# Performance work log

Hardware: AMD Instinct MI355X
Metric: run time of the kernel (lower is better)

The kernel has to match this reference:

```python
import jax, jax.numpy as jnp
import numpy as np

B, N, D = 2, 2048, 1024
H = 16
HD = D // H
SCALE = HD ** -0.5


def setup_inputs() -> dict:
    key = jax.random.key(0)
    k1, k2, kw, kb = jax.random.split(key, 4)
    x1 = jax.random.normal(k1, (B, N, D), dtype=jnp.float32)
    x2 = jax.random.normal(k2, (B, N, D), dtype=jnp.float32)
    # fused qkv linear: torch nn.Linear(dim, 3*dim): W [3D, D], b [3D]
    bound = 1.0 / np.sqrt(D)
    qkv_w = jax.random.uniform(kw, (3 * D, D), minval=-bound, maxval=bound, dtype=jnp.float32)
    qkv_b = jax.random.uniform(kb, (3 * D,), minval=-bound, maxval=bound, dtype=jnp.float32)
    return {"x1": x1, "x2": x2, "qkv_w": qkv_w, "qkv_b": qkv_b}


def reference(x1, x2, qkv_w, qkv_b):
    # qkv projections (only q from x1 and k,v from x2 are used by the module)
    q1 = (jnp.einsum('bnd,ed->bne', x1, qkv_w[:D]) + qkv_b[:D])
    k2 = (jnp.einsum('bnd,ed->bne', x2, qkv_w[D:2 * D]) + qkv_b[D:2 * D])
    v2 = (jnp.einsum('bnd,ed->bne', x2, qkv_w[2 * D:]) + qkv_b[2 * D:])
    # [B, H, N, HD]
    q1 = q1.reshape(B, N, H, HD).transpose(0, 2, 1, 3)
    k2 = k2.reshape(B, N, H, HD).transpose(0, 2, 1, 3)
    v2 = v2.reshape(B, N, H, HD).transpose(0, 2, 1, 3)
    # explicit QK^T -> softmax -> AV (materializes [B,H,N,N] like the original)
    scores = jnp.einsum('bhqd,bhkd->bhqk', q1, k2) * SCALE
    attn = jax.nn.softmax(scores, axis=-1)
    out = jnp.einsum('bhqk,bhkd->bhqd', attn, v2)
    # [B, N, D]; note original module skips out_proj (never applied in forward)
    return out.transpose(0, 2, 1, 3).reshape(B, N, D)
```

## Files before the change

kernel.cpp:

```cpp
#include <hip/hip_runtime.h>
#include <cstdint>
#include <cstddef>

#define B_   2
#define N_   2048
#define D_   1024
#define H_   16
#define HD_  64
#define QSCALE_ 0.18033688011112042f

typedef unsigned short u16;
typedef unsigned int   u32;
typedef __attribute__((ext_vector_type(8))) short short8;
typedef __attribute__((ext_vector_type(4))) float f32x4;
typedef __attribute__((ext_vector_type(4))) float fl4;
typedef __attribute__((ext_vector_type(4))) unsigned short us4;

__device__ __forceinline__ u16 f2bf(float f) {
  u32 u = __builtin_bit_cast(u32, f);
  u += 0x7fffu + ((u >> 16) & 1u);
  return (u16)(u >> 16);
}

__device__ __forceinline__ void gload16(const void* g, void* l) {
  typedef __attribute__((address_space(1))) unsigned int gu32;
  typedef __attribute__((address_space(3))) unsigned int lu32;
  __builtin_amdgcn_global_load_lds((gu32*)g, (lu32*)l, 16, 0, 0);
}

__global__ void convert_kernel(const fl4* __restrict__ x1, const fl4* __restrict__ x2,
                               const fl4* __restrict__ w,
                               us4* __restrict__ o1, us4* __restrict__ o2,
                               us4* __restrict__ ow) {
  const int NX = (B_ * N_ * D_) / 4;
  const int NW = (3 * D_ * D_) / 4;
  int stride = gridDim.x * blockDim.x;
  for (int i = blockIdx.x * blockDim.x + threadIdx.x; i < NX; i += stride) {
    fl4 a = x1[i];
    us4 r; r.x = f2bf(a.x); r.y = f2bf(a.y); r.z = f2bf(a.z); r.w = f2bf(a.w);
    o1[i] = r;
    fl4 b = x2[i];
    us4 s; s.x = f2bf(b.x); s.y = f2bf(b.y); s.z = f2bf(b.z); s.w = f2bf(b.w);
    o2[i] = s;
    if (i < NW) {
      fl4 c = w[i];
      us4 t; t.x = f2bf(c.x); t.y = f2bf(c.y); t.z = f2bf(c.z); t.w = f2bf(c.w);
      ow[i] = t;
    }
  }
}

__global__ __launch_bounds__(256) void qkv_gemm(
    const u16* __restrict__ x1b, const u16* __restrict__ x2b,
    const u16* __restrict__ wb, const float* __restrict__ bias,
    u16* __restrict__ Qb, u16* __restrict__ Kb, u16* __restrict__ Vcb) {
  const int z = blockIdx.z;
  const u16* X = (z == 0) ? x1b : x2b;
  const u16* W = wb + (size_t)z * D_ * D_;
  const float* bz = bias + z * D_;
  const int m0 = blockIdx.y * 128;
  const int e0 = blockIdx.x * 128;
  const int tid = threadIdx.x;
  const int lane = tid & 63;
  const int w = tid >> 6;
  const int wr = w >> 1, wc = w & 1;
  const int col = lane & 15, quad = lane >> 4;

  __shared__ __align__(16) u16 As[128 * 32];
  __shared__ __align__(16) u16 Bs[128 * 32];
  __shared__ __align__(16) u16 Tb[4][16 * 72];

  f32x4 acc[4][4] = {};

  int off0 = w * 2048 + lane * 16;
  int row0 = off0 >> 6;
  int ke0  = (off0 & 63) >> 1;
  int off1 = off0 + 1024;
  int row1 = off1 >> 6;
  int ke1  = (off1 & 63) >> 1;

  const u16* gA0 = X + (size_t)(m0 + row0) * D_ + ke0;
  const u16* gA1 = X + (size_t)(m0 + row1) * D_ + ke1;
  const u16* gB0 = W + (size_t)(e0 + row0) * D_ + ke0;
  const u16* gB1 = W + (size_t)(e0 + row1) * D_ + ke1;
  u16* lA0 = &As[w * 1024];
  u16* lA1 = &As[w * 1024 + 512];
  u16* lB0 = &Bs[w * 1024];
  u16* lB1 = &Bs[w * 1024 + 512];

  for (int k0 = 0; k0 < D_; k0 += 32) {
    __syncthreads();
    gload16(gA0 + k0, lA0);
    gload16(gA1 + k0, lA1);
    gload16(gB0 + k0, lB0);
    gload16(gB1 + k0, lB1);
    __syncthreads();

    short8 a[4], b[4];
#pragma unroll
    for (int i = 0; i < 4; ++i)
      a[i] = *(const short8*)&As[(wr * 64 + i * 16 + col) * 32 + quad * 8];
#pragma unroll
    for (int j = 0; j < 4; ++j)
      b[j] = *(const short8*)&Bs[(wc * 64 + j * 16 + col) * 32 + quad * 8];
#pragma unroll
    for (int i = 0; i < 4; ++i)
#pragma unroll
      for (int j = 0; j < 4; ++j)
        acc[i][j] = __builtin_amdgcn_mfma_f32_16x16x32_bf16(a[i], b[j], acc[i][j], 0, 0, 0);
  }

  if (z == 2) {
#pragma unroll
    for (int j = 0; j < 4; ++j) {
      int eg = e0 + wc * 64 + j * 16 + col;
      float bj = bz[eg];
      int h = eg >> 6, d = eg & 63;
#pragma unroll
      for (int i = 0; i < 4; ++i) {
        int m  = m0 + wr * 64 + i * 16 + quad * 4;
        int bb = m >> 11;
        int nc = (m & (N_ - 1)) >> 6;
        int no = i * 16 + quad * 4;
        int p  = (no >> 3) ^ (d & 7);
        us4 pk;
#pragma unroll
        for (int r = 0; r < 4; ++r) pk[r] = f2bf(acc[i][j][r] + bj);
        *(us4*)&Vcb[((((size_t)bb * H_ + h) * (N_ / 64) + nc) * HD_ + d) * 64
                    + p * 8 + (no & 7)] = pk;
      }
    }
  } else {
    u16* Tw = Tb[w];
    const int h = (e0 + wc * 64) >> 6;
    const int mb = m0 + wr * 64;
    const int bb = mb >> 11;
    const int nb = mb & (N_ - 1);
    float bjv[4];
#pragma unroll
    for (int j = 0; j < 4; ++j) bjv[j] = bz[e0 + wc * 64 + j * 16 + col];

    const int trow = lane >> 2;
    const int tchk = lane & 3;
#pragma unroll
    for (int i = 0; i < 4; ++i) {
#pragma unroll
      for (int j = 0; j < 4; ++j)
#pragma unroll
        for (int r = 0; r < 4; ++r) {
          float v = acc[i][j][r] + bjv[j];
          if (z == 0) v *= QSCALE_;
          Tw[(quad * 4 + r) * 72 + j * 16 + col] = f2bf(v);
        }
      __asm__ volatile("" ::: "memory");
      int n = nb + i * 16 + trow;
      size_t base = (((size_t)bb * H_ + h) * N_ + n) * HD_;
#pragma unroll
      for (int pass = 0; pass < 2; ++pass) {
        short8 vv = *(const short8*)&Tw[trow * 72 + tchk * 8 + pass * 32];
        if (z == 0) {
          *(short8*)&Qb[base + tchk * 8 + pass * 32] = vv;
        } else {
          int p = (tchk + 4 * pass) ^ (n & 7);
          *(short8*)&Kb[base + p * 8] = vv;
        }
      }
      __asm__ volatile("" ::: "memory");
    }
  }
}

__global__ __launch_bounds__(256, 3) void attn_kernel(
    const u16* __restrict__ Qb, const u16* __restrict__ Kb,
    const u16* __restrict__ Vcb, float* __restrict__ out) {
  const int bh = blockIdx.y;
  const int bb = bh >> 4, h = bh & 15;
  const int q0 = blockIdx.x * 128;
  const int tid = threadIdx.x;
  const int lane = tid & 63;
  const int w = tid >> 6;
  const int col = lane & 15, quad = lane >> 4;

  const u16* __restrict__ Q  = Qb  + ((size_t)bh << 17);
  const u16* __restrict__ Kg = Kb  + ((size_t)bh << 17);
  const u16* __restrict__ Vg = Vcb + ((size_t)bh << 17);

  __shared__ __align__(16) u16 Ks[2][64 * 64];
  __shared__ __align__(16) u16 Vs[2][64 * 64];
  __shared__ __align__(16) u16 P[4][32 * 72];
  u16* Pw = P[w];

  short8 qa[2][2];
#pragma unroll
  for (int m = 0; m < 2; ++m) {
    int qrow = q0 + w * 32 + m * 16 + col;
    qa[m][0] = *(const short8*)&Q[qrow * HD_ + quad * 8];
    qa[m][1] = *(const short8*)&Q[qrow * HD_ + 32 + quad * 8];
  }

  const int soff = (tid >> 3) * 64 + (tid & 7) * 8;

  f32x4 accO[2][4] = {};
  float lsum[2][4] = {};
  const int swz = col & 7;

  {
    const u16* gk = Kg + soff;
    const u16* gv = Vg + soff;
    gload16(gk,        &Ks[0][soff]);
    gload16(gk + 2048, &Ks[0][soff + 2048]);
    gload16(gv,        &Vs[0][soff]);
    gload16(gv + 2048, &Vs[0][soff + 2048]);
  }

  for (int it = 0; it < N_ / 64; ++it) {
    const int buf = it & 1;
    __syncthreads();
    if (it + 1 < N_ / 64) {
      const int k0 = (it + 1) * 64;
      const u16* gk = Kg + k0 * 64 + soff;
      const u16* gv = Vg + k0 * 64 + soff;
      gload16(gk,        &Ks[buf ^ 1][soff]);
      gload16(gk + 2048, &Ks[buf ^ 1][soff + 2048]);
      gload16(gv,        &Vs[buf ^ 1][soff]);
      gload16(gv + 2048, &Vs[buf ^ 1][soff + 2048]);
    }

    const u16* Kt = Ks[buf];
    f32x4 s[2][4] = {};
#pragma unroll
    for (int jn = 0; jn < 4; ++jn) {
      int base = (jn * 16 + col) * 64 + ((quad ^ swz) * 8);
      short8 kb0 = *(const short8*)&Kt[base];
      short8 kb1 = *(const short8*)&Kt[base ^ 32];
#pragma unroll
      for (int m = 0; m < 2; ++m) {
        s[m][jn] = __builtin_amdgcn_mfma_f32_16x16x32_bf16(qa[m][0], kb0, s[m][jn], 0, 0, 0);
        s[m][jn] = __builtin_amdgcn_mfma_f32_16x16x32_bf16(qa[m][1], kb1, s[m][jn], 0, 0, 0);
      }
    }

#pragma unroll
    for (int m = 0; m < 2; ++m)
#pragma unroll
      for (int jn = 0; jn < 4; ++jn)
#pragma unroll
        for (int r = 0; r < 4; ++r) {
          float e = exp2f(s[m][jn][r]);
          lsum[m][r] += e;
          Pw[(m * 16 + quad * 4 + r) * 72 + jn * 16 + col] =
              (u16)(__builtin_bit_cast(u32, e) >> 16);
        }
    __asm__ volatile("" ::: "memory");
    short8 pa[2][2];
#pragma unroll
    for (int m = 0; m < 2; ++m) {
      pa[m][0] = *(const short8*)&Pw[(m * 16 + col) * 72 + quad * 8];
      pa[m][1] = *(const short8*)&Pw[(m * 16 + col) * 72 + 32 + quad * 8];
    }
    __asm__ volatile("" ::: "memory");

    const u16* Vt = Vs[buf];
#pragma unroll
    for (int jd = 0; jd < 4; ++jd) {
      int base = (jd * 16 + col) * 64 + ((quad ^ swz) * 8);
      short8 vb0 = *(const short8*)&Vt[base];
      short8 vb1 = *(const short8*)&Vt[base ^ 32];
#pragma unroll
      for (int m = 0; m < 2; ++m) {
        accO[m][jd] = __builtin_amdgcn_mfma_f32_16x16x32_bf16(pa[m][0], vb0, accO[m][jd], 0, 0, 0);
        accO[m][jd] = __builtin_amdgcn_mfma_f32_16x16x32_bf16(pa[m][1], vb1, accO[m][jd], 0, 0, 0);
      }
    }
  }

#pragma unroll
  for (int m = 0; m < 2; ++m)
#pragma unroll
    for (int r = 0; r < 4; ++r) {
      float v = lsum[m][r];
      v += __shfl_xor(v, 1);
      v += __shfl_xor(v, 2);
      v += __shfl_xor(v, 4);
      v += __shfl_xor(v, 8);
      lsum[m][r] = 1.0f / v;
    }

#pragma unroll
  for (int m = 0; m < 2; ++m)
#pragma unroll
    for (int jd = 0; jd < 4; ++jd)
#pragma unroll
      for (int r = 0; r < 4; ++r) {
        int n = q0 + w * 32 + m * 16 + quad * 4 + r;
        int e = h * HD_ + jd * 16 + col;
        out[((size_t)bb * N_ + n) * D_ + e] = accO[m][jd][r] * lsum[m][r];
      }
}

extern "C" void kernel_launch(void* const* d_in, const int* in_sizes, int n_in,
                              void* d_out, int out_size, void* d_ws, size_t ws_size,
                              hipStream_t stream) {
  const float* x1 = (const float*)d_in[0];
  const float* x2 = (const float*)d_in[1];
  const float* qw = (const float*)d_in[2];
  const float* qb = (const float*)d_in[3];
  float* out = (float*)d_out;

  u16* ws   = (u16*)d_ws;
  u16* x1b  = ws;
  u16* x2b  = ws + 4194304;
  u16* wb   = ws + 8388608;
  u16* Qbf  = ws + 11534336;
  u16* Kbf  = ws + 15728640;
  u16* Vcb  = ws + 19922944;
  if (ws_size < (size_t)24117248 * 2) return;

  convert_kernel<<<dim3(1024), dim3(256), 0, stream>>>(
      (const fl4*)x1, (const fl4*)x2, (const fl4*)qw,
      (us4*)x1b, (us4*)x2b, (us4*)wb);

  qkv_gemm<<<dim3(8, 32, 3), dim3(256), 0, stream>>>(
      x1b, x2b, wb, qb, Qbf, Kbf, Vcb);

  attn_kernel<<<dim3(16, 32), dim3(256), 0, stream>>>(Qbf, Kbf, Vcb, out);
}
```

Measured before the change: 208.4 us.

## Use two waves with 64 query rows each in attention, and native exp2

The attention block shrinks from four waves to two. Each wave now covers 64 query rows (4 m-tiles), so every K/V fragment read from shared memory feeds twice as many MFMAs. The K/V tile loads are redistributed across 128 threads, and exp2f is replaced by the hardware v_exp_f32 instruction to skip libm range handling. In exchange, register pressure roughly doubles for the accumulators, and there are fewer waves per block to hide latency, which the launch bounds reflect.

```diff
diff --git a/kernel.cpp b/kernel.cpp
--- a/kernel.cpp
+++ b/kernel.cpp
@@ -20,6 +20,16 @@
   u32 u = __builtin_bit_cast(u32, f);
   u += 0x7fffu + ((u >> 16) & 1u);
   return (u16)(u >> 16);
+}
+
+__device__ __forceinline__ float fexp2(float x) {
+#if __has_builtin(__builtin_amdgcn_exp2f)
+  return __builtin_amdgcn_exp2f(x);
+#else
+  float r;
+  asm("v_exp_f32 %0, %1" : "=v"(r) : "v"(x));
+  return r;
+#endif
 }
 
 __device__ __forceinline__ void gload16(const void* g, void* l) {
@@ -170,7 +180,7 @@
   }
 }
 
-__global__ __launch_bounds__(256, 3) void attn_kernel(
+__global__ __launch_bounds__(128, 2) void attn_kernel(
     const u16* __restrict__ Qb, const u16* __restrict__ Kb,
     const u16* __restrict__ Vcb, float* __restrict__ out) {
   const int bh = blockIdx.y;
@@ -187,30 +197,27 @@
 
   __shared__ __align__(16) u16 Ks[2][64 * 64];
   __shared__ __align__(16) u16 Vs[2][64 * 64];
-  __shared__ __align__(16) u16 P[4][32 * 72];
+  __shared__ __align__(16) u16 P[2][64 * 72];
   u16* Pw = P[w];
 
-  short8 qa[2][2];
-#pragma unroll
-  for (int m = 0; m < 2; ++m) {
-    int qrow = q0 + w * 32 + m * 16 + col;
+  short8 qa[4][2];
+#pragma unroll
+  for (int m = 0; m < 4; ++m) {
+    int qrow = q0 + w * 64 + m * 16 + col;
     qa[m][0] = *(const short8*)&Q[qrow * HD_ + quad * 8];
     qa[m][1] = *(const short8*)&Q[qrow * HD_ + 32 + quad * 8];
   }
 
-  const int soff = (tid >> 3) * 64 + (tid & 7) * 8;
-
-  f32x4 accO[2][4] = {};
-  float lsum[2][4] = {};
+  const int soff = tid * 8;
+
+  f32x4 accO[4][4] = {};
+  float lsum[4][4] = {};
   const int swz = col & 7;
 
-  {
-    const u16* gk = Kg + soff;
-    const u16* gv = Vg + soff;
-    gload16(gk,        &Ks[0][soff]);
-    gload16(gk + 2048, &Ks[0][soff + 2048]);
-    gload16(gv,        &Vs[0][soff]);
-    gload16(gv + 2048, &Vs[0][soff + 2048]);
+#pragma unroll
+  for (int s = 0; s < 4; ++s) {
+    gload16(Kg + soff + s * 1024, &Ks[0][soff + s * 1024]);
+    gload16(Vg + soff + s * 1024, &Vs[0][soff + s * 1024]);
   }
 
   for (int it = 0; it < N_ / 64; ++it) {
@@ -220,41 +227,42 @@
       const int k0 = (it + 1) * 64;
       const u16* gk = Kg + k0 * 64 + soff;
       const u16* gv = Vg + k0 * 64 + soff;
-      gload16(gk,        &Ks[buf ^ 1][soff]);
-      gload16(gk + 2048, &Ks[buf ^ 1][soff + 2048]);
-      gload16(gv,        &Vs[buf ^ 1][soff]);
-      gload16(gv + 2048, &Vs[buf ^ 1][soff + 2048]);
+#pragma unroll
+      for (int s = 0; s < 4; ++s) {
+        gload16(gk + s * 1024, &Ks[buf ^ 1][soff + s * 1024]);
+        gload16(gv + s * 1024, &Vs[buf ^ 1][soff + s * 1024]);
+      }
     }
 
     const u16* Kt = Ks[buf];
-    f32x4 s[2][4] = {};
+    f32x4 s[4][4] = {};
 #pragma unroll
     for (int jn = 0; jn < 4; ++jn) {
       int base = (jn * 16 + col) * 64 + ((quad ^ swz) * 8);
       short8 kb0 = *(const short8*)&Kt[base];
       short8 kb1 = *(const short8*)&Kt[base ^ 32];
 #pragma unroll
-      for (int m = 0; m < 2; ++m) {
+      for (int m = 0; m < 4; ++m) {
         s[m][jn] = __builtin_amdgcn_mfma_f32_16x16x32_bf16(qa[m][0], kb0, s[m][jn], 0, 0, 0);
         s[m][jn] = __builtin_amdgcn_mfma_f32_16x16x32_bf16(qa[m][1], kb1, s[m][jn], 0, 0, 0);
       }
     }
 
 #pragma unroll
-    for (int m = 0; m < 2; ++m)
+    for (int m = 0; m < 4; ++m)
 #pragma unroll
       for (int jn = 0; jn < 4; ++jn)
 #pragma unroll
         for (int r = 0; r < 4; ++r) {
-          float e = exp2f(s[m][jn][r]);
+          float e = fexp2(s[m][jn][r]);
           lsum[m][r] += e;
           Pw[(m * 16 + quad * 4 + r) * 72 + jn * 16 + col] =
               (u16)(__builtin_bit_cast(u32, e) >> 16);
         }
     __asm__ volatile("" ::: "memory");
-    short8 pa[2][2];
-#pragma unroll
-    for (int m = 0; m < 2; ++m) {
+    short8 pa[4][2];
+#pragma unroll
+    for (int m = 0; m < 4; ++m) {
       pa[m][0] = *(const short8*)&Pw[(m * 16 + col) * 72 + quad * 8];
       pa[m][1] = *(const short8*)&Pw[(m * 16 + col) * 72 + 32 + quad * 8];
     }
@@ -267,7 +275,7 @@
       short8 vb0 = *(const short8*)&Vt[base];
       short8 vb1 = *(const short8*)&Vt[base ^ 32];
 #pragma unroll
-      for (int m = 0; m < 2; ++m) {
+      for (int m = 0; m < 4; ++m) {
         accO[m][jd] = __builtin_amdgcn_mfma_f32_16x16x32_bf16(pa[m][0], vb0, accO[m][jd], 0, 0, 0);
         accO[m][jd] = __builtin_amdgcn_mfma_f32_16x16x32_bf16(pa[m][1], vb1, accO[m][jd], 0, 0, 0);
       }
@@ -275,7 +283,7 @@
   }
 
 #pragma unroll
-  for (int m = 0; m < 2; ++m)
+  for (int m = 0; m < 4; ++m)
 #pragma unroll
     for (int r = 0; r < 4; ++r) {
       float v = lsum[m][r];
@@ -287,12 +295,12 @@
     }
 
 #pragma unroll
-  for (int m = 0; m < 2; ++m)
+  for (int m = 0; m < 4; ++m)
 #pragma unroll
     for (int jd = 0; jd < 4; ++jd)
 #pragma unroll
       for (int r = 0; r < 4; ++r) {
-        int n = q0 + w * 32 + m * 16 + quad * 4 + r;
+        int n = q0 + w * 64 + m * 16 + quad * 4 + r;
         int e = h * HD_ + jd * 16 + col;
         out[((size_t)bb * N_ + n) * D_ + e] = accO[m][jd][r] * lsum[m][r];
       }
@@ -323,5 +331,5 @@
   qkv_gemm<<<dim3(8, 32, 3), dim3(256), 0, stream>>>(
       x1b, x2b, wb, qb, Qbf, Kbf, Vcb);
 
-  attn_kernel<<<dim3(16, 32), dim3(256), 0, stream>>>(Qbf, Kbf, Vcb, out);
-}
+  attn_kernel<<<dim3(16, 32), dim3(128), 0, stream>>>(Qbf, Kbf, Vcb, out);
+}
```

Result: slower. 223.9 us (+7.4%).
